# Performance work log

Hardware: AMD Instinct MI355X
Metric: run time of the kernel (lower is better)

Reference implementation:

```python
import jax, jax.numpy as jnp
import numpy as np

N = 100000   # nodes
E = 1600000  # edges
G = 256      # graphs in batch
C_IN = 128
D = 64
EPS = 1e-5
SLOPE = 0.01  # torch LeakyReLU default


def gcn_conv(h_x, src, dst, w_edge, W, b):
    """GCNConv: linear -> symmetric-normalized scatter aggregation (+ self loops) -> bias."""
    n = h_x.shape[0]
    h = h_x @ W                                   # [N, D]
    # add self loops with weight 1
    loop = jnp.arange(n, dtype=src.dtype)
    s = jnp.concatenate([src, loop])
    d = jnp.concatenate([dst, loop])
    w = jnp.concatenate([w_edge, jnp.ones((n,), h_x.dtype)])
    deg = jax.ops.segment_sum(w, d, num_segments=n)  # degree on target nodes
    dinv = jnp.where(deg > 0, jax.lax.rsqrt(jnp.maximum(deg, 1e-12)), 0.0)
    norm = dinv[s] * w * dinv[d]                  # [E+N]
    msg = h[s] * norm[:, None]                    # gather + scale
    out = jax.ops.segment_sum(msg, d, num_segments=n)
    return out + b


def batch_norm(h, gamma, beta):
    mean = jnp.mean(h, axis=0)
    var = jnp.mean((h - mean) ** 2, axis=0)       # biased var (training-mode BN)
    return (h - mean) * jax.lax.rsqrt(var + EPS) * gamma + beta


def setup_inputs() -> dict:
    key = jax.random.key(0)
    ks = jax.random.split(key, 16)
    inp = {
        "x": jax.random.normal(ks[0], (N, C_IN), jnp.float32),
        "edge_index": jax.random.randint(ks[1], (2, E), 0, N, jnp.int32),
        "batch": jnp.sort(jax.random.randint(ks[2], (N,), 0, G, jnp.int32)),
        "edge_attr": jax.random.uniform(ks[3], (E,), jnp.float32),
        "W0": jax.random.normal(ks[4], (C_IN, D), jnp.float32) * 0.05,
        "b0": jnp.zeros((D,), jnp.float32),
        "g0": jnp.ones((D,), jnp.float32),
        "be0": jnp.zeros((D,), jnp.float32),
        "W1": jax.random.normal(ks[5], (D, D), jnp.float32) * 0.05,
        "b1": jnp.zeros((D,), jnp.float32),
        "g1": jnp.ones((D,), jnp.float32),
        "be1": jnp.zeros((D,), jnp.float32),
        "W2": jax.random.normal(ks[6], (D, D), jnp.float32) * 0.05,
        "b2": jnp.zeros((D,), jnp.float32),
        "W3": jax.random.normal(ks[7], (D, D), jnp.float32) * 0.05,
        "b3": jnp.zeros((D,), jnp.float32),
        "Wfc": jax.random.normal(ks[8], (2 * D, 1), jnp.float32) * 0.05,
        "bfc": jnp.zeros((1,), jnp.float32),
    }
    return inp


def reference(x, edge_index, batch, edge_attr,
              W0, b0, g0, be0, W1, b1, g1, be1, W2, b2, W3, b3, Wfc, bfc):
    src, dst = edge_index[0], edge_index[1]
    lrelu = lambda h: jax.nn.leaky_relu(h, SLOPE)

    h = lrelu(batch_norm(gcn_conv(x, src, dst, edge_attr, W0, b0), g0, be0))
    h = lrelu(batch_norm(gcn_conv(h, src, dst, edge_attr, W1, b1), g1, be1))
    h = lrelu(gcn_conv(h, src, dst, edge_attr, W2, b2))  # dropout is identity in eval
    h = lrelu(gcn_conv(h, src, dst, edge_attr, W3, b3))

    mx = jax.ops.segment_max(h, batch, num_segments=G)
    sm = jax.ops.segment_sum(h, batch, num_segments=G)
    cnt = jax.ops.segment_sum(jnp.ones((N,), h.dtype), batch, num_segments=G)
    mean = sm / jnp.maximum(cnt, 1.0)[:, None]
    pooled = jnp.concatenate([mx, mean], axis=1)   # [G, 2D]
    return pooled @ Wfc + bfc                      # [G, 1]
```

## Files before the change

### kernel.cpp

```cpp
#include <hip/hip_runtime.h>
#include <math.h>

#define LRELU_SLOPE 0.01f
#define BN_EPS 1e-5f
#define WQ_SCALE 1048576.0f
#define WQ_INV   9.5367431640625e-7f

static inline int ceil_div(int a, int b) { return (a + b - 1) / b; }

typedef _Float16 f16;
typedef f16 h4_t __attribute__((ext_vector_type(4)));
typedef f16 h8_t __attribute__((ext_vector_type(8)));
typedef float f32x4 __attribute__((ext_vector_type(4)));

__device__ __forceinline__ unsigned short f2bf(float f) {
  unsigned int u = __float_as_uint(f);
  u = u + 0x7FFFu + ((u >> 16) & 1u);
  return (unsigned short)(u >> 16);
}
#define BF2F(u) __uint_as_float(((unsigned int)(u)) << 16)

__launch_bounds__(1024)
__global__ void b1_hist(const int* __restrict__ ei, int* __restrict__ histT,
                        int E, int chunk, int nbuck) {
  __shared__ unsigned int hist[1024];
  const int t = threadIdx.x;
  const int blk = blockIdx.x;
  hist[t] = 0;
  __syncthreads();
  const int e0 = blk * chunk;
  const int e1 = min(e0 + chunk, E);
  for (int e = e0 + t; e < e1; e += 1024) {
    int d = ei[E + e];
    atomicAdd(&hist[d >> 7], 1u);
  }
  __syncthreads();
  if (t < nbuck) histT[(size_t)t * 256 + blk] = (int)hist[t];
}

__global__ void scan1i(const int* __restrict__ in, int* __restrict__ out,
                       int* __restrict__ bsum, int n) {
  __shared__ int lds[256];
  const int t = threadIdx.x;
  const int base = blockIdx.x * 1024 + t * 4;
  int v0 = 0, v1 = 0, v2 = 0, v3 = 0;
  if (base + 0 < n) v0 = in[base + 0];
  if (base + 1 < n) v1 = in[base + 1];
  if (base + 2 < n) v2 = in[base + 2];
  if (base + 3 < n) v3 = in[base + 3];
  int s = v0 + v1 + v2 + v3;
  lds[t] = s;
  __syncthreads();
#pragma unroll
  for (int off = 1; off < 256; off <<= 1) {
    int y = 0;
    if (t >= off) y = lds[t - off];
    __syncthreads();
    if (t >= off) lds[t] += y;
    __syncthreads();
  }
  int incl = lds[t];
  int excl = incl - s;
  if (base + 0 < n) out[base + 0] = excl;
  if (base + 1 < n) out[base + 1] = excl + v0;
  if (base + 2 < n) out[base + 2] = excl + v0 + v1;
  if (base + 3 < n) out[base + 3] = excl + v0 + v1 + v2;
  if (t == 255) bsum[blockIdx.x] = incl;
}

__global__ void scan2i(int* __restrict__ bsum, int nb) {
  __shared__ int lds[256];
  int t = threadIdx.x;
  int v = (t < nb) ? bsum[t] : 0;
  lds[t] = v;
  __syncthreads();
#pragma unroll
  for (int off = 1; off < 256; off <<= 1) {
    int y = 0;
    if (t >= off) y = lds[t - off];
    __syncthreads();
    if (t >= off) lds[t] += y;
    __syncthreads();
  }
  if (t < nb) bsum[t] = lds[t] - v;
}

__global__ void scan3i(int* __restrict__ data, const int* __restrict__ bscan, int n) {
  int i = blockIdx.x * blockDim.x + threadIdx.x;
  if (i < n) data[i] += bscan[i >> 10];
}

__launch_bounds__(1024)
__global__ void b3_scatter(const int* __restrict__ ei, const float* __restrict__ w,
                           const int* __restrict__ histS,
                           unsigned long long* __restrict__ bucketed,
                           int E, int chunk, int nbuck) {
  __shared__ unsigned int cursor[1024];
  const int t = threadIdx.x;
  const int blk = blockIdx.x;
  cursor[t] = (t < nbuck) ? (unsigned int)histS[(size_t)t * 256 + blk] : 0u;
  __syncthreads();
  const int e0 = blk * chunk;
  const int e1 = min(e0 + chunk, E);
  for (int e = e0 + t; e < e1; e += 1024) {
    int s = ei[e];
    int d = ei[E + e];
    unsigned int pos = atomicAdd(&cursor[d >> 7], 1u);
    unsigned long long p = ((unsigned long long)(unsigned int)(d & 127) << 57) |
                           ((unsigned long long)(unsigned int)s << 32) |
                           (unsigned long long)__float_as_uint(w[e]);
    bucketed[pos] = p;
  }
}

__launch_bounds__(256)
__global__ void c1_degree(const unsigned long long* __restrict__ bucketed,
                          const int* __restrict__ histS,
                          int* __restrict__ rowstart, float* __restrict__ dinv,
                          int N, int E, int nbuck) {
  __shared__ unsigned int cnt[128], wsum[128];
  __shared__ int sc[128];
  const int t = threadIdx.x;
  const int b = blockIdx.x;
  if (t < 128) { cnt[t] = 0; wsum[t] = 0; }
  __syncthreads();
  const int r0 = histS[(size_t)b * 256];
  const int r1 = (b + 1 < nbuck) ? histS[(size_t)(b + 1) * 256] : E;
  for (int r = r0 + t; r < r1; r += 256) {
    unsigned long long p = bucketed[r];
    int d7 = (int)(p >> 57);
    float wv = __uint_as_float((unsigned int)p);
    atomicAdd(&cnt[d7], 1u);
    atomicAdd(&wsum[d7], (unsigned int)__float2uint_rn(wv * WQ_SCALE));
  }
  __syncthreads();
  if (t < 128) sc[t] = (int)cnt[t];
  __syncthreads();
#pragma unroll
  for (int off = 1; off < 128; off <<= 1) {
    int y = 0;
    if (t < 128 && t >= off) y = sc[t - off];
    __syncthreads();
    if (t < 128 && t >= off) sc[t] += y;
    __syncthreads();
  }
  if (t < 128) {
    int node = (b << 7) + t;
    if (node < N) {
      rowstart[node] = r0 + sc[t] - (int)cnt[t];
      float deg = 1.0f + (float)wsum[t] * WQ_INV;
      dinv[node] = rsqrtf(deg);
    }
  }
  if (b == 0 && t == 0) rowstart[N] = E;
}

__launch_bounds__(256)
__global__ void c2_fill(const unsigned long long* __restrict__ bucketed,
                        const int* __restrict__ histS,
                        const int* __restrict__ rowstart, const float* __restrict__ dinv,
                        unsigned long long* __restrict__ colval,
                        int N, int E, int nbuck) {
  __shared__ unsigned int cursor[128];
  const int t = threadIdx.x;
  const int b = blockIdx.x;
  if (t < 128) {
    int node = (b << 7) + t;
    cursor[t] = (node < N) ? (unsigned int)rowstart[node] : 0u;
  }
  __syncthreads();
  const int r0 = histS[(size_t)b * 256];
  const int r1 = (b + 1 < nbuck) ? histS[(size_t)(b + 1) * 256] : E;
  for (int r = r0 + t; r < r1; r += 256) {
    unsigned long long p = bucketed[r];
    int d7 = (int)(p >> 57);
    int s = (int)((p >> 32) & 0x1FFFFFF);
    float wv = __uint_as_float((unsigned int)p);
    unsigned int pos = atomicAdd(&cursor[d7], 1u);
    float v = wv * dinv[s];
    colval[pos] = ((unsigned long long)(unsigned int)s << 32) |
                  (unsigned long long)__float_as_uint(v);
  }
}

template <int K, int BN>
__launch_bounds__(256, 4)
__global__ void k_gemm(const float* __restrict__ X, const float* __restrict__ W,
                       unsigned short* __restrict__ H16,
                       const float* __restrict__ s, const float* __restrict__ ss,
                       const float* __restrict__ g, const float* __restrict__ be,
                       int N) {
  constexpr int KP = K + 8;
  constexpr int KQ = K / 4;
  __shared__ f16 Xl[64 * KP];
  __shared__ f16 Wt[64 * KP];
  __shared__ float scaleC[64], shiftC[64];
  const int t = threadIdx.x;
  const int n0 = blockIdx.x * 64;

  if (BN) {
    if (t < 64) {
      float invN = 1.0f / (float)N;
      float mean = s[t] * invN;
      float var = ss[t] * invN - mean * mean;
      float sc = g[t] * rsqrtf(var + BN_EPS);
      scaleC[t] = sc;
      shiftC[t] = be[t] - mean * sc;
    }
    __syncthreads();
  }

  for (int idx = t; idx < 64 * KQ; idx += 256) {
    int row = idx / KQ;
    int kq = idx % KQ;
    int gn = n0 + row;
    float4 v = make_float4(0.f, 0.f, 0.f, 0.f);
    if (gn < N) v = *(const float4*)(X + (size_t)gn * K + 4 * kq);
    if (BN) {
      int c = 4 * kq;
      float a;
      a = v.x * scaleC[c + 0] + shiftC[c + 0]; v.x = (a > 0.f) ? a : LRELU_SLOPE * a;
      a = v.y * scaleC[c + 1] + shiftC[c + 1]; v.y = (a > 0.f) ? a : LRELU_SLOPE * a;
      a = v.z * scaleC[c + 2] + shiftC[c + 2]; v.z = (a > 0.f) ? a : LRELU_SLOPE * a;
      a = v.w * scaleC[c + 3] + shiftC[c + 3]; v.w = (a > 0.f) ? a : LRELU_SLOPE * a;
    }
    h4_t hv = { (f16)v.x, (f16)v.y, (f16)v.z, (f16)v.w };
    *(h4_t*)(Xl + row * KP + 4 * kq) = hv;
  }
  for (int idx = t; idx < K * 16; idx += 256) {
    int k = idx >> 4;
    int c4 = idx & 15;
    float4 wv = *(const float4*)(W + (size_t)k * 64 + 4 * c4);
    Wt[(4 * c4 + 0) * KP + k] = (f16)wv.x;
    Wt[(4 * c4 + 1) * KP + k] = (f16)wv.y;
    Wt[(4 * c4 + 2) * KP + k] = (f16)wv.z;
    Wt[(4 * c4 + 3) * KP + k] = (f16)wv.w;
  }
  __syncthreads();

  const int lane = t & 63;
  const int wv = t >> 6;
  const int fr = lane & 15;
  const int fc = lane >> 4;

  f32x4 acc0 = {0.f, 0.f, 0.f, 0.f};
  f32x4 acc1 = {0.f, 0.f, 0.f, 0.f};
  f32x4 acc2 = {0.f, 0.f, 0.f, 0.f};
  f32x4 acc3 = {0.f, 0.f, 0.f, 0.f};

  const f16* ap = Xl + (16 * wv + fr) * KP + 8 * fc;
  const f16* bp0 = Wt + (0 + fr) * KP + 8 * fc;
  const f16* bp1 = Wt + (16 + fr) * KP + 8 * fc;
  const f16* bp2 = Wt + (32 + fr) * KP + 8 * fc;
  const f16* bp3 = Wt + (48 + fr) * KP + 8 * fc;

#pragma unroll
  for (int kt = 0; kt < K; kt += 32) {
    h8_t a = *(const h8_t*)(ap + kt);
    acc0 = __builtin_amdgcn_mfma_f32_16x16x32_f16(a, *(const h8_t*)(bp0 + kt), acc0, 0, 0, 0);
    acc1 = __builtin_amdgcn_mfma_f32_16x16x32_f16(a, *(const h8_t*)(bp1 + kt), acc1, 0, 0, 0);
    acc2 = __builtin_amdgcn_mfma_f32_16x16x32_f16(a, *(const h8_t*)(bp2 + kt), acc2, 0, 0, 0);
    acc3 = __builtin_amdgcn_mfma_f32_16x16x32_f16(a, *(const h8_t*)(bp3 + kt), acc3, 0, 0, 0);
  }

#pragma unroll
  for (int r = 0; r < 4; ++r) {
    int node = n0 + 16 * wv + 4 * fc + r;
    if (node < N) {
      size_t base = (size_t)node * 64 + fr;
      H16[base + 0]  = f2bf(acc0[r]);
      H16[base + 16] = f2bf(acc1[r]);
      H16[base + 32] = f2bf(acc2[r]);
      H16[base + 48] = f2bf(acc3[r]);
    }
  }
}

#define AGG_GATH(cv) (*(const ushort4*)(h16 + ((size_t)((cv) >> 32)) * 64 + lane * 4))
#define AGG_FMA(a, cv, h)                                     \
  {                                                           \
    float v_ = __uint_as_float((unsigned int)(cv));           \
    (a).x += v_ * BF2F((h).x); (a).y += v_ * BF2F((h).y);     \
    (a).z += v_ * BF2F((h).z); (a).w += v_ * BF2F((h).w);     \
  }
template <int STATS, int LRELU>
__launch_bounds__(256, 4)
__global__ void k_agg(const unsigned short* __restrict__ h16, float* __restrict__ hout,
                      const float* __restrict__ bias, const float* __restrict__ dinv,
                      const int* __restrict__ rowstart,
                      const unsigned long long* __restrict__ colval,
                      float* __restrict__ partial, int N) {
  __shared__ float4 rs[STATS ? 256 : 1];
  __shared__ float4 rq[STATS ? 256 : 1];
  const int t = threadIdx.x;
  const int grp = t >> 4;
  const int lane = t & 15;
  const int d = blockIdx.x * 16 + grp;
  const bool valid = (d < N);
  int r0 = 0, r1 = 0;
  if (valid) { r0 = rowstart[d]; r1 = rowstart[d + 1]; }
  float4 a0 = make_float4(0.f, 0.f, 0.f, 0.f);
  float4 a1 = make_float4(0.f, 0.f, 0.f, 0.f);
  float4 a2 = make_float4(0.f, 0.f, 0.f, 0.f);
  float4 a3 = make_float4(0.f, 0.f, 0.f, 0.f);
  int r = r0;
  for (; r + 16 <= r1; r += 16) {
    unsigned long long cv0 = colval[r + 0];
    unsigned long long cv1 = colval[r + 1];
    unsigned long long cv2 = colval[r + 2];
    unsigned long long cv3 = colval[r + 3];
    unsigned long long cv4 = colval[r + 4];
    unsigned long long cv5 = colval[r + 5];
    unsigned long long cv6 = colval[r + 6];
    unsigned long long cv7 = colval[r + 7];
    unsigned long long cv8 = colval[r + 8];
    unsigned long long cv9 = colval[r + 9];
    unsigned long long cva = colval[r + 10];
    unsigned long long cvb = colval[r + 11];
    unsigned long long cvc = colval[r + 12];
    unsigned long long cvd = colval[r + 13];
    unsigned long long cve = colval[r + 14];
    unsigned long long cvf = colval[r + 15];
    ushort4 h0 = AGG_GATH(cv0);
    ushort4 h1 = AGG_GATH(cv1);
    ushort4 h2 = AGG_GATH(cv2);
    ushort4 h3 = AGG_GATH(cv3);
    ushort4 h4 = AGG_GATH(cv4);
    ushort4 h5 = AGG_GATH(cv5);
    ushort4 h6 = AGG_GATH(cv6);
    ushort4 h7 = AGG_GATH(cv7);
    ushort4 h8 = AGG_GATH(cv8);
    ushort4 h9 = AGG_GATH(cv9);
    ushort4 ha = AGG_GATH(cva);
    ushort4 hb = AGG_GATH(cvb);
    ushort4 hc = AGG_GATH(cvc);
    ushort4 hd = AGG_GATH(cvd);
    ushort4 he = AGG_GATH(cve);
    ushort4 hf = AGG_GATH(cvf);
    AGG_FMA(a0, cv0, h0); AGG_FMA(a1, cv1, h1);
    AGG_FMA(a2, cv2, h2); AGG_FMA(a3, cv3, h3);
    AGG_FMA(a0, cv4, h4); AGG_FMA(a1, cv5, h5);
    AGG_FMA(a2, cv6, h6); AGG_FMA(a3, cv7, h7);
    AGG_FMA(a0, cv8, h8); AGG_FMA(a1, cv9, h9);
    AGG_FMA(a2, cva, ha); AGG_FMA(a3, cvb, hb);
    AGG_FMA(a0, cvc, hc); AGG_FMA(a1, cvd, hd);
    AGG_FMA(a2, cve, he); AGG_FMA(a3, cvf, hf);
  }
  for (; r + 8 <= r1; r += 8) {
    unsigned long long cv0 = colval[r + 0];
    unsigned long long cv1 = colval[r + 1];
    unsigned long long cv2 = colval[r + 2];
    unsigned long long cv3 = colval[r + 3];
    unsigned long long cv4 = colval[r + 4];
    unsigned long long cv5 = colval[r + 5];
    unsigned long long cv6 = colval[r + 6];
    unsigned long long cv7 = colval[r + 7];
    ushort4 h0 = AGG_GATH(cv0);
    ushort4 h1 = AGG_GATH(cv1);
    ushort4 h2 = AGG_GATH(cv2);
    ushort4 h3 = AGG_GATH(cv3);
    ushort4 h4 = AGG_GATH(cv4);
    ushort4 h5 = AGG_GATH(cv5);
    ushort4 h6 = AGG_GATH(cv6);
    ushort4 h7 = AGG_GATH(cv7);
    AGG_FMA(a0, cv0, h0); AGG_FMA(a1, cv1, h1);
    AGG_FMA(a2, cv2, h2); AGG_FMA(a3, cv3, h3);
    AGG_FMA(a0, cv4, h4); AGG_FMA(a1, cv5, h5);
    AGG_FMA(a2, cv6, h6); AGG_FMA(a3, cv7, h7);
  }
  for (; r + 4 <= r1; r += 4) {
    unsigned long long cv0 = colval[r + 0];
    unsigned long long cv1 = colval[r + 1];
    unsigned long long cv2 = colval[r + 2];
    unsigned long long cv3 = colval[r + 3];
    ushort4 h0 = AGG_GATH(cv0);
    ushort4 h1 = AGG_GATH(cv1);
    ushort4 h2 = AGG_GATH(cv2);
    ushort4 h3 = AGG_GATH(cv3);
    AGG_FMA(a0, cv0, h0); AGG_FMA(a1, cv1, h1);
    AGG_FMA(a2, cv2, h2); AGG_FMA(a3, cv3, h3);
  }
  for (; r < r1; ++r) {
    unsigned long long cv = colval[r];
    ushort4 hv = AGG_GATH(cv);
    AGG_FMA(a0, cv, hv);
  }
  float4 acc;
  acc.x = (a0.x + a1.x) + (a2.x + a3.x);
  acc.y = (a0.y + a1.y) + (a2.y + a3.y);
  acc.z = (a0.z + a1.z) + (a2.z + a3.z);
  acc.w = (a0.w + a1.w) + (a2.w + a3.w);
  float di = valid ? dinv[d] : 0.f;
  float di2 = di * di;
  ushort4 hd4 = make_ushort4(0, 0, 0, 0);
  if (valid) hd4 = *(const ushort4*)(h16 + (size_t)d * 64 + lane * 4);
  float4 b4 = *(const float4*)(bias + lane * 4);
  float4 o;
  o.x = di * acc.x + di2 * BF2F(hd4.x) + b4.x;
  o.y = di * acc.y + di2 * BF2F(hd4.y) + b4.y;
  o.z = di * acc.z + di2 * BF2F(hd4.z) + b4.z;
  o.w = di * acc.w + di2 * BF2F(hd4.w) + b4.w;
  if (LRELU) {
    o.x = (o.x > 0.f) ? o.x : LRELU_SLOPE * o.x;
    o.y = (o.y > 0.f) ? o.y : LRELU_SLOPE * o.y;
    o.z = (o.z > 0.f) ? o.z : LRELU_SLOPE * o.z;
    o.w = (o.w > 0.f) ? o.w : LRELU_SLOPE * o.w;
  }
  if (!valid) o = make_float4(0.f, 0.f, 0.f, 0.f);
  if (valid) *(float4*)(hout + (size_t)d * 64 + lane * 4) = o;

  if (STATS) {
    rs[t] = o;
    rq[t] = make_float4(o.x * o.x, o.y * o.y, o.z * o.z, o.w * o.w);
    __syncthreads();
#pragma unroll
    for (int st = 8; st >= 1; st >>= 1) {
      if ((t >> 4) < st) {
        float4 sa = rs[t], sb = rs[t + st * 16];
        float4 qa = rq[t], qb = rq[t + st * 16];
        rs[t] = make_float4(sa.x + sb.x, sa.y + sb.y, sa.z + sb.z, sa.w + sb.w);
        rq[t] = make_float4(qa.x + qb.x, qa.y + qb.y, qa.z + qb.z, qa.w + qb.w);
      }
      __syncthreads();
    }
    if (t < 16) {
      float4 sv = rs[t], qv = rq[t];
      float* ps = partial + (size_t)blockIdx.x * 128 + 4 * t;
      ps[0] = sv.x; ps[1] = sv.y; ps[2] = sv.z; ps[3] = sv.w;
      ps[64] = qv.x; ps[65] = qv.y; ps[66] = qv.z; ps[67] = qv.w;
    }
  }
}

__global__ void k_stats_reduce(const float* __restrict__ partial, float* __restrict__ s,
                               float* __restrict__ ss, int nb) {
  __shared__ float red[256];
  const int c = blockIdx.x;
  const int t = threadIdx.x;
  float a = 0.f;
  for (int b = t; b < nb; b += 256) a += partial[(size_t)b * 128 + c];
  red[t] = a;
  __syncthreads();
  for (int st = 128; st >= 1; st >>= 1) {
    if (t < st) red[t] += red[t + st];
    __syncthreads();
  }
  if (t == 0) {
    if (c < 64) s[c] = red[0];
    else ss[c - 64] = red[0];
  }
}

__global__ void k_gbounds(const int* __restrict__ batch, int* __restrict__ gstart,
                          int N, int G) {
  int i = blockIdx.x * blockDim.x + threadIdx.x;
  if (i >= N) return;
  int b = batch[i];
  int prev = (i == 0) ? -1 : batch[i - 1];
  for (int g = prev + 1; g <= b; ++g) gstart[g] = i;
  if (i == N - 1) {
    for (int g = b + 1; g <= G; ++g) gstart[g] = N;
  }
}

__launch_bounds__(256)
__global__ void k_pool(const float* __restrict__ h, const int* __restrict__ gstart,
                       const float* __restrict__ Wfc, const float* __restrict__ bfc,
                       float* __restrict__ out, int G) {
  __shared__ float lmx[256], lsm[256], red[128];
  const int g = blockIdx.x;
  const int t = threadIdx.x;
  const int c = t & 63;
  const int sub = t >> 6;
  const int n0 = gstart[g];
  const int n1 = gstart[g + 1];
  float mx = -INFINITY, sm = 0.f;
  for (int n = n0 + sub; n < n1; n += 4) {
    float v = h[(size_t)n * 64 + c];
    mx = fmaxf(mx, v);
    sm += v;
  }
  lmx[t] = mx;
  lsm[t] = sm;
  __syncthreads();
  if (t < 64) {
    mx = fmaxf(fmaxf(lmx[t], lmx[t + 64]), fmaxf(lmx[t + 128], lmx[t + 192]));
    sm = lsm[t] + lsm[t + 64] + lsm[t + 128] + lsm[t + 192];
    float cntf = (float)(n1 - n0);
    float mean = sm / fmaxf(cntf, 1.0f);
    red[t] = mx * Wfc[t];
    red[t + 64] = mean * Wfc[64 + t];
  }
  __syncthreads();
  for (int st = 64; st >= 1; st >>= 1) {
    if (t < st) red[t] += red[t + st];
    __syncthreads();
  }
  if (t == 0) out[g] = red[0] + bfc[0];
}

extern "C" void kernel_launch(void* const* d_in, const int* in_sizes, int n_in,
                              void* d_out, int out_size, void* d_ws, size_t ws_size,
                              hipStream_t stream) {
  const float* x = (const float*)d_in[0];
  const int* ei = (const int*)d_in[1];
  const int* batch = (const int*)d_in[2];
  const float* eattr = (const float*)d_in[3];
  const float* W0 = (const float*)d_in[4];
  const float* b0 = (const float*)d_in[5];
  const float* g0 = (const float*)d_in[6];
  const float* be0 = (const float*)d_in[7];
  const float* W1 = (const float*)d_in[8];
  const float* b1 = (const float*)d_in[9];
  const float* g1 = (const float*)d_in[10];
  const float* be1 = (const float*)d_in[11];
  const float* W2 = (const float*)d_in[12];
  const float* b2 = (const float*)d_in[13];
  const float* W3 = (const float*)d_in[14];
  const float* b3 = (const float*)d_in[15];
  const float* Wfc = (const float*)d_in[16];
  const float* bfc = (const float*)d_in[17];
  float* out = (float*)d_out;

  const int N = in_sizes[2];
  const int E = in_sizes[3];
  const int CIN = in_sizes[0] / N;
  const int G = out_size;
  const int nbuck = ceil_div(N, 128);
  const int chunk = ceil_div(E, 256);
  const int M = nbuck * 256;
  const int nag = ceil_div(N, 16);

  size_t off = 0;
  auto alloc = [&](size_t bytes) -> void* {
    void* p = (char*)d_ws + off;
    off += (bytes + 255) & ~(size_t)255;
    return p;
  };
  int* histT = (int*)alloc((size_t)1024 * 256 * 4);
  int* histS = (int*)alloc((size_t)1024 * 256 * 4);
  int* bsum = (int*)alloc(1024 * 4);
  unsigned long long* bucketed = (unsigned long long*)alloc((size_t)E * 8);
  float* dinv = (float*)alloc((size_t)N * 4);
  int* rowstart = (int*)alloc((size_t)(N + 1) * 4);
  unsigned long long* colval = (unsigned long long*)alloc((size_t)E * 8);
  float* A = (float*)alloc((size_t)N * 64 * 4);
  float* B = (float*)alloc((size_t)N * 64 * 4);
  unsigned short* H16 = (unsigned short*)alloc((size_t)N * 64 * 2);
  float* sums = (float*)alloc(256 * 4);
  float* partial = (float*)alloc((size_t)nag * 128 * 4);
  int* gstart = (int*)alloc((size_t)(G + 1) * 4);
  (void)ws_size; (void)n_in; (void)CIN;

  b1_hist<<<256, 1024, 0, stream>>>(ei, histT, E, chunk, nbuck);
  const int nbs = ceil_div(M, 1024);
  scan1i<<<nbs, 256, 0, stream>>>(histT, histS, bsum, M);
  scan2i<<<1, 256, 0, stream>>>(bsum, nbs);
  scan3i<<<ceil_div(M, 256), 256, 0, stream>>>(histS, bsum, M);
  b3_scatter<<<256, 1024, 0, stream>>>(ei, eattr, histS, bucketed, E, chunk, nbuck);
  c1_degree<<<nbuck, 256, 0, stream>>>(bucketed, histS, rowstart, dinv, N, E, nbuck);
  c2_fill<<<nbuck, 256, 0, stream>>>(bucketed, histS, rowstart, dinv, colval, N, E, nbuck);
  k_gbounds<<<ceil_div(N, 256), 256, 0, stream>>>(batch, gstart, N, G);

  k_gemm<128, 0><<<ceil_div(N, 64), 256, 0, stream>>>(x, W0, H16, nullptr, nullptr, nullptr, nullptr, N);
  k_agg<1, 0><<<nag, 256, 0, stream>>>(H16, B, b0, dinv, rowstart, colval, partial, N);
  k_stats_reduce<<<128, 256, 0, stream>>>(partial, sums + 0, sums + 64, nag);

  k_gemm<64, 1><<<ceil_div(N, 64), 256, 0, stream>>>(B, W1, H16, sums + 0, sums + 64, g0, be0, N);
  k_agg<1, 0><<<nag, 256, 0, stream>>>(H16, A, b1, dinv, rowstart, colval, partial, N);
  k_stats_reduce<<<128, 256, 0, stream>>>(partial, sums + 128, sums + 192, nag);

  k_gemm<64, 1><<<ceil_div(N, 64), 256, 0, stream>>>(A, W2, H16, sums + 128, sums + 192, g1, be1, N);
  k_agg<0, 1><<<nag, 256, 0, stream>>>(H16, B, b2, dinv, rowstart, colval, nullptr, N);

  k_gemm<64, 0><<<ceil_div(N, 64), 256, 0, stream>>>(B, W3, H16, nullptr, nullptr, nullptr, nullptr, N);
  k_agg<0, 1><<<nag, 256, 0, stream>>>(H16, A, b3, dinv, rowstart, colval, nullptr, N);

  k_pool<<<G, 256, 0, stream>>>(A, gstart, Wfc, bfc, out, G);
}
```

Before: 450.4 us.

## Replace bucketed CSR construction with global-atomic count, scan and fill

Builds the CSR adjacency by counting in-degree and weighted degree per node with global atomics, scanning counts, then filling columns via per-node atomic cursors. This removes the two-level bucket sort and its intermediate buffer and several passes. It adds heavy global atomic contention, randomly ordered writes, and nondeterministic edge order and float degree sums. It also drops the 16-wide unroll and the occupancy hint in the aggregation kernel.

```diff
diff --git a/kernel.cpp b/kernel.cpp
--- a/kernel.cpp
+++ b/kernel.cpp
@@ -3,8 +3,6 @@
 
 #define LRELU_SLOPE 0.01f
 #define BN_EPS 1e-5f
-#define WQ_SCALE 1048576.0f
-#define WQ_INV   9.5367431640625e-7f
 
 static inline int ceil_div(int a, int b) { return (a + b - 1) / b; }
 
@@ -20,22 +18,20 @@
 }
 #define BF2F(u) __uint_as_float(((unsigned int)(u)) << 16)
 
-__launch_bounds__(1024)
-__global__ void b1_hist(const int* __restrict__ ei, int* __restrict__ histT,
-                        int E, int chunk, int nbuck) {
-  __shared__ unsigned int hist[1024];
-  const int t = threadIdx.x;
-  const int blk = blockIdx.x;
-  hist[t] = 0;
-  __syncthreads();
-  const int e0 = blk * chunk;
-  const int e1 = min(e0 + chunk, E);
-  for (int e = e0 + t; e < e1; e += 1024) {
-    int d = ei[E + e];
-    atomicAdd(&hist[d >> 7], 1u);
-  }
-  __syncthreads();
-  if (t < nbuck) histT[(size_t)t * 256 + blk] = (int)hist[t];
+__global__ void k_zero(unsigned int* __restrict__ p, int n) {
+  int i = blockIdx.x * blockDim.x + threadIdx.x;
+  if (i < n) p[i] = 0u;
+}
+
+__launch_bounds__(256)
+__global__ void k_deg(const int* __restrict__ ei, const float* __restrict__ w,
+                      unsigned int* __restrict__ cnt, float* __restrict__ degw,
+                      int E) {
+  int e = blockIdx.x * blockDim.x + threadIdx.x;
+  if (e >= E) return;
+  int d = ei[E + e];
+  atomicAdd(&cnt[d], 1u);
+  atomicAdd(&degw[d], w[e]);
 }
 
 __global__ void scan1i(const int* __restrict__ in, int* __restrict__ out,
@@ -90,97 +86,28 @@
   if (i < n) data[i] += bscan[i >> 10];
 }
 
-__launch_bounds__(1024)
-__global__ void b3_scatter(const int* __restrict__ ei, const float* __restrict__ w,
-                           const int* __restrict__ histS,
-                           unsigned long long* __restrict__ bucketed,
-                           int E, int chunk, int nbuck) {
-  __shared__ unsigned int cursor[1024];
-  const int t = threadIdx.x;
-  const int blk = blockIdx.x;
-  cursor[t] = (t < nbuck) ? (unsigned int)histS[(size_t)t * 256 + blk] : 0u;
-  __syncthreads();
-  const int e0 = blk * chunk;
-  const int e1 = min(e0 + chunk, E);
-  for (int e = e0 + t; e < e1; e += 1024) {
-    int s = ei[e];
-    int d = ei[E + e];
-    unsigned int pos = atomicAdd(&cursor[d >> 7], 1u);
-    unsigned long long p = ((unsigned long long)(unsigned int)(d & 127) << 57) |
-                           ((unsigned long long)(unsigned int)s << 32) |
-                           (unsigned long long)__float_as_uint(w[e]);
-    bucketed[pos] = p;
-  }
+__global__ void k_dinv(const float* __restrict__ degw, float* __restrict__ dinv,
+                       const int* __restrict__ rowstart, unsigned int* __restrict__ cursor,
+                       int N, int E) {
+  int i = blockIdx.x * blockDim.x + threadIdx.x;
+  if (i >= N) return;
+  dinv[i] = rsqrtf(1.0f + degw[i]);
+  cursor[i] = (unsigned int)rowstart[i];
+  if (i == 0) ((int*)rowstart)[N] = E;
 }
 
 __launch_bounds__(256)
-__global__ void c1_degree(const unsigned long long* __restrict__ bucketed,
-                          const int* __restrict__ histS,
-                          int* __restrict__ rowstart, float* __restrict__ dinv,
-                          int N, int E, int nbuck) {
-  __shared__ unsigned int cnt[128], wsum[128];
-  __shared__ int sc[128];
-  const int t = threadIdx.x;
-  const int b = blockIdx.x;
-  if (t < 128) { cnt[t] = 0; wsum[t] = 0; }
-  __syncthreads();
-  const int r0 = histS[(size_t)b * 256];
-  const int r1 = (b + 1 < nbuck) ? histS[(size_t)(b + 1) * 256] : E;
-  for (int r = r0 + t; r < r1; r += 256) {
-    unsigned long long p = bucketed[r];
-    int d7 = (int)(p >> 57);
-    float wv = __uint_as_float((unsigned int)p);
-    atomicAdd(&cnt[d7], 1u);
-    atomicAdd(&wsum[d7], (unsigned int)__float2uint_rn(wv * WQ_SCALE));
-  }
-  __syncthreads();
-  if (t < 128) sc[t] = (int)cnt[t];
-  __syncthreads();
-#pragma unroll
-  for (int off = 1; off < 128; off <<= 1) {
-    int y = 0;
-    if (t < 128 && t >= off) y = sc[t - off];
-    __syncthreads();
-    if (t < 128 && t >= off) sc[t] += y;
-    __syncthreads();
-  }
-  if (t < 128) {
-    int node = (b << 7) + t;
-    if (node < N) {
-      rowstart[node] = r0 + sc[t] - (int)cnt[t];
-      float deg = 1.0f + (float)wsum[t] * WQ_INV;
-      dinv[node] = rsqrtf(deg);
-    }
-  }
-  if (b == 0 && t == 0) rowstart[N] = E;
-}
-
-__launch_bounds__(256)
-__global__ void c2_fill(const unsigned long long* __restrict__ bucketed,
-                        const int* __restrict__ histS,
-                        const int* __restrict__ rowstart, const float* __restrict__ dinv,
-                        unsigned long long* __restrict__ colval,
-                        int N, int E, int nbuck) {
-  __shared__ unsigned int cursor[128];
-  const int t = threadIdx.x;
-  const int b = blockIdx.x;
-  if (t < 128) {
-    int node = (b << 7) + t;
-    cursor[t] = (node < N) ? (unsigned int)rowstart[node] : 0u;
-  }
-  __syncthreads();
-  const int r0 = histS[(size_t)b * 256];
-  const int r1 = (b + 1 < nbuck) ? histS[(size_t)(b + 1) * 256] : E;
-  for (int r = r0 + t; r < r1; r += 256) {
-    unsigned long long p = bucketed[r];
-    int d7 = (int)(p >> 57);
-    int s = (int)((p >> 32) & 0x1FFFFFF);
-    float wv = __uint_as_float((unsigned int)p);
-    unsigned int pos = atomicAdd(&cursor[d7], 1u);
-    float v = wv * dinv[s];
-    colval[pos] = ((unsigned long long)(unsigned int)s << 32) |
-                  (unsigned long long)__float_as_uint(v);
-  }
+__global__ void k_fill(const int* __restrict__ ei, const float* __restrict__ w,
+                       const float* __restrict__ dinv, unsigned int* __restrict__ cursor,
+                       unsigned long long* __restrict__ colval, int E) {
+  int e = blockIdx.x * blockDim.x + threadIdx.x;
+  if (e >= E) return;
+  int s = ei[e];
+  int d = ei[E + e];
+  unsigned int pos = atomicAdd(&cursor[d], 1u);
+  float v = w[e] * dinv[s];
+  colval[pos] = ((unsigned long long)(unsigned int)s << 32) |
+                (unsigned long long)__float_as_uint(v);
 }
 
 template <int K, int BN>
@@ -284,7 +211,7 @@
     (a).z += v_ * BF2F((h).z); (a).w += v_ * BF2F((h).w);     \
   }
 template <int STATS, int LRELU>
-__launch_bounds__(256, 4)
+__launch_bounds__(256)
 __global__ void k_agg(const unsigned short* __restrict__ h16, float* __restrict__ hout,
                       const float* __restrict__ bias, const float* __restrict__ dinv,
                       const int* __restrict__ rowstart,
@@ -304,48 +231,6 @@
   float4 a2 = make_float4(0.f, 0.f, 0.f, 0.f);
   float4 a3 = make_float4(0.f, 0.f, 0.f, 0.f);
   int r = r0;
-  for (; r + 16 <= r1; r += 16) {
-    unsigned long long cv0 = colval[r + 0];
-    unsigned long long cv1 = colval[r + 1];
-    unsigned long long cv2 = colval[r + 2];
-    unsigned long long cv3 = colval[r + 3];
-    unsigned long long cv4 = colval[r + 4];
-    unsigned long long cv5 = colval[r + 5];
-    unsigned long long cv6 = colval[r + 6];
-    unsigned long long cv7 = colval[r + 7];
-    unsigned long long cv8 = colval[r + 8];
-    unsigned long long cv9 = colval[r + 9];
-    unsigned long long cva = colval[r + 10];
-    unsigned long long cvb = colval[r + 11];
-    unsigned long long cvc = colval[r + 12];
-    unsigned long long cvd = colval[r + 13];
-    unsigned long long cve = colval[r + 14];
-    unsigned long long cvf = colval[r + 15];
-    ushort4 h0 = AGG_GATH(cv0);
-    ushort4 h1 = AGG_GATH(cv1);
-    ushort4 h2 = AGG_GATH(cv2);
-    ushort4 h3 = AGG_GATH(cv3);
-    ushort4 h4 = AGG_GATH(cv4);
-    ushort4 h5 = AGG_GATH(cv5);
-    ushort4 h6 = AGG_GATH(cv6);
-    ushort4 h7 = AGG_GATH(cv7);
-    ushort4 h8 = AGG_GATH(cv8);
-    ushort4 h9 = AGG_GATH(cv9);
-    ushort4 ha = AGG_GATH(cva);
-    ushort4 hb = AGG_GATH(cvb);
-    ushort4 hc = AGG_GATH(cvc);
-    ushort4 hd = AGG_GATH(cvd);
-    ushort4 he = AGG_GATH(cve);
-    ushort4 hf = AGG_GATH(cvf);
-    AGG_FMA(a0, cv0, h0); AGG_FMA(a1, cv1, h1);
-    AGG_FMA(a2, cv2, h2); AGG_FMA(a3, cv3, h3);
-    AGG_FMA(a0, cv4, h4); AGG_FMA(a1, cv5, h5);
-    AGG_FMA(a2, cv6, h6); AGG_FMA(a3, cv7, h7);
-    AGG_FMA(a0, cv8, h8); AGG_FMA(a1, cv9, h9);
-    AGG_FMA(a2, cva, ha); AGG_FMA(a3, cvb, hb);
-    AGG_FMA(a0, cvc, hc); AGG_FMA(a1, cvd, hd);
-    AGG_FMA(a2, cve, he); AGG_FMA(a3, cvf, hf);
-  }
   for (; r + 8 <= r1; r += 8) {
     unsigned long long cv0 = colval[r + 0];
     unsigned long long cv1 = colval[r + 1];
@@ -526,9 +411,6 @@
   const int E = in_sizes[3];
   const int CIN = in_sizes[0] / N;
   const int G = out_size;
-  const int nbuck = ceil_div(N, 128);
-  const int chunk = ceil_div(E, 256);
-  const int M = nbuck * 256;
   const int nag = ceil_div(N, 16);
 
   size_t off = 0;
@@ -537,10 +419,10 @@
     off += (bytes + 255) & ~(size_t)255;
     return p;
   };
-  int* histT = (int*)alloc((size_t)1024 * 256 * 4);
-  int* histS = (int*)alloc((size_t)1024 * 256 * 4);
+  unsigned int* cnt = (unsigned int*)alloc((size_t)N * 4);
+  float* degw = (float*)alloc((size_t)N * 4);
+  unsigned int* cursor = (unsigned int*)alloc((size_t)N * 4);
   int* bsum = (int*)alloc(1024 * 4);
-  unsigned long long* bucketed = (unsigned long long*)alloc((size_t)E * 8);
   float* dinv = (float*)alloc((size_t)N * 4);
   int* rowstart = (int*)alloc((size_t)(N + 1) * 4);
   unsigned long long* colval = (unsigned long long*)alloc((size_t)E * 8);
@@ -552,14 +434,14 @@
   int* gstart = (int*)alloc((size_t)(G + 1) * 4);
   (void)ws_size; (void)n_in; (void)CIN;
 
-  b1_hist<<<256, 1024, 0, stream>>>(ei, histT, E, chunk, nbuck);
-  const int nbs = ceil_div(M, 1024);
-  scan1i<<<nbs, 256, 0, stream>>>(histT, histS, bsum, M);
+  k_zero<<<ceil_div(2 * N, 256), 256, 0, stream>>>(cnt, 2 * N);
+  k_deg<<<ceil_div(E, 256), 256, 0, stream>>>(ei, eattr, cnt, degw, E);
+  const int nbs = ceil_div(N, 1024);
+  scan1i<<<nbs, 256, 0, stream>>>((const int*)cnt, rowstart, bsum, N);
   scan2i<<<1, 256, 0, stream>>>(bsum, nbs);
-  scan3i<<<ceil_div(M, 256), 256, 0, stream>>>(histS, bsum, M);
-  b3_scatter<<<256, 1024, 0, stream>>>(ei, eattr, histS, bucketed, E, chunk, nbuck);
-  c1_degree<<<nbuck, 256, 0, stream>>>(bucketed, histS, rowstart, dinv, N, E, nbuck);
-  c2_fill<<<nbuck, 256, 0, stream>>>(bucketed, histS, rowstart, dinv, colval, N, E, nbuck);
+  scan3i<<<ceil_div(N, 256), 256, 0, stream>>>(rowstart, bsum, N);
+  k_dinv<<<ceil_div(N, 256), 256, 0, stream>>>(degw, dinv, rowstart, cursor, N, E);
+  k_fill<<<ceil_div(E, 256), 256, 0, stream>>>(ei, eattr, dinv, cursor, colval, E);
   k_gbounds<<<ceil_div(N, 256), 256, 0, stream>>>(batch, gstart, N, G);
 
   k_gemm<128, 0><<<ceil_div(N, 64), 256, 0, stream>>>(x, W0, H16, nullptr, nullptr, nullptr, nullptr, N);
```

Measured after the change: 625.7 us. 1.39x slower.
